# Performance work log

Measured on AMD Instinct MI355X. Metric: run time of the kernel, lower is better.

## Reference

```python
import jax, jax.numpy as jnp
import numpy as np

N_NODES = 20000

def _gcn_conv(x, W, b, src, dst, n):
    # PyG GCNConv: add self-loops, symmetric normalization D^-1/2 (A+I) D^-1/2, then XW + b
    h = x @ W                                   # [n, out]
    loop = jnp.arange(n, dtype=src.dtype)
    s = jnp.concatenate([src, loop])            # sources incl. self-loops
    d = jnp.concatenate([dst, loop])            # targets incl. self-loops
    deg = jax.ops.segment_sum(jnp.ones_like(d, dtype=h.dtype), d, num_segments=n)
    dinv = jnp.where(deg > 0, jax.lax.rsqrt(deg), 0.0)
    norm = dinv[s] * dinv[d]                    # [E+n]
    msg = h[s] * norm[:, None]                  # gather + scale
    out = jax.ops.segment_sum(msg, d, num_segments=n)  # scatter-add
    return out + b


def setup_inputs() -> dict:
    key = jax.random.key(0)
    ks = jax.random.split(key, 12)
    n, text_dim, hidden, ncls = N_NODES, 768, 128, 4
    mel_flat = 128 * 128
    E = 640000
    def lin(k, fan_in, fan_out):
        bound = 1.0 / np.sqrt(fan_in)
        kw, kb = jax.random.split(k)
        W = jax.random.uniform(kw, (fan_in, fan_out), jnp.float32, -bound, bound)
        b = jax.random.uniform(kb, (fan_out,), jnp.float32, -bound, bound)
        return W, b
    W_mel, b_mel = lin(ks[0], mel_flat, hidden)
    W_cat, b_cat = lin(ks[1], text_dim + hidden, hidden)
    W1, b1 = lin(ks[2], hidden, hidden)
    W2, b2 = lin(ks[3], hidden, ncls)
    return {
        "text": jax.random.normal(ks[4], (n, text_dim), jnp.float32),
        "mel": jax.random.normal(ks[5], (n, 128, 128), jnp.float32),
        "edge_index": jax.random.randint(ks[6], (2, E), 0, n, jnp.int32),
        "W_mel": W_mel, "b_mel": b_mel,
        "W_cat": W_cat, "b_cat": b_cat,
        "W1": W1, "b1": b1,
        "W2": W2, "b2": b2,
    }


def reference(text, mel, edge_index, W_mel, b_mel, W_cat, b_cat, W1, b1, W2, b2):
    n = text.shape[0]
    src, dst = edge_index[0], edge_index[1]
    m = mel.reshape(n, -1)                      # flatten [N, 128*128]
    m = jax.nn.relu(m @ W_mel + b_mel)          # [N, hidden]
    x = jnp.concatenate([text, m], axis=1)      # [N, text_dim + hidden]
    x = jax.nn.relu(x @ W_cat + b_cat)          # [N, hidden]
    x = jax.nn.relu(_gcn_conv(x, W1, b1, src, dst, n))
    x = _gcn_conv(x, W2, b2, src, dst, n)       # [N, num_classes]
    return x
```

## Files before the change

kernel.cpp:

```cpp
#include <hip/hip_runtime.h>
#include <hip/hip_bf16.h>
#include <cstdint>

typedef float f32x4 __attribute__((ext_vector_type(4)));
typedef __bf16 bf16x8 __attribute__((ext_vector_type(8)));
typedef __bf16 bf16x4 __attribute__((ext_vector_type(4)));

#define HID 128

__global__ void pack_b_frag(const float* __restrict__ W, __bf16* __restrict__ Bf, int kiters) {
    int idx = blockIdx.x * 256 + threadIdx.x;
    int total = kiters * 512;
    if (idx >= total) return;
    int lane = idx & 63;
    int nf = (idx >> 6) & 7;
    int ki = idx >> 9;
    int n = nf * 16 + (lane & 15);
    int kb = ki * 32 + ((lane >> 4) * 8);
    bf16x8 v;
#pragma unroll
    for (int j = 0; j < 8; ++j) v[j] = (__bf16)W[(size_t)(kb + j) * HID + n];
    *reinterpret_cast<bf16x8*>(Bf + (size_t)idx * 8) = v;
}

__global__ __launch_bounds__(256, 2) void gemm_mel_ks(
    const float* __restrict__ A0,
    const __bf16* __restrict__ Bf,
    float* __restrict__ part)
{
    const int tid = threadIdx.x;
    const int lane = tid & 63;
    const int wv = tid >> 6;
    const int quarter = blockIdx.x / 625;
    const int row_base = (blockIdx.x - quarter * 625) * 32;
    const int rif = lane & 15;
    const int kg = lane >> 4;
    const int s0 = quarter * 8;

    __shared__ __align__(16) char ldsb[65536];

    f32x4 zero = {0.f, 0.f, 0.f, 0.f};
    f32x4 acc[2][8];
#pragma unroll
    for (int i = 0; i < 2; ++i)
#pragma unroll
        for (int j = 0; j < 8; ++j) acc[i][j] = zero;

    const bf16x8* __restrict__ BfV = reinterpret_cast<const bf16x8*>(Bf);

    f32x4 st[16];

    auto stage_load = [&](int s) {
#pragma unroll
        for (int j = 0; j < 16; ++j) {
            int seg = wv * 16 + j;
            int row = seg >> 1, halfseg = seg & 1;
            const float* gp = A0 + (size_t)(row_base + row) * 16384 + s * 512 + halfseg * 256 + (lane << 2);
            st[j] = __builtin_nontemporal_load(reinterpret_cast<const f32x4*>(gp));
        }
    };
    auto stage_write = [&](int buf) {
#pragma unroll
        for (int j = 0; j < 16; ++j) {
            int seg = wv * 16 + j;
            int row = seg >> 1, halfseg = seg & 1;
            int byte = row * 1024 + ((halfseg * 512 + lane * 8) ^ ((row & 7) << 4)) + buf * 32768;
            bf16x4 v;
            v[0] = (__bf16)st[j][0]; v[1] = (__bf16)st[j][1];
            v[2] = (__bf16)st[j][2]; v[3] = (__bf16)st[j][3];
            *reinterpret_cast<bf16x4*>(ldsb + byte) = v;
        }
    };
    auto compute2 = [&](int cur, int s, int kt0) {
#pragma unroll
        for (int kt = kt0; kt < kt0 + 2; ++kt) {
            bf16x8 af[2];
#pragma unroll
            for (int mi = 0; mi < 2; ++mi) {
                int row = mi * 16 + rif;
                int byte = row * 1024 + ((wv * 256 + kt * 64 + kg * 16) ^ ((rif & 7) << 4)) + cur * 32768;
                af[mi] = *reinterpret_cast<const bf16x8*>(ldsb + byte);
            }
            int ki = s * 16 + wv * 4 + kt;
            const bf16x8* bp = BfV + (size_t)ki * 512 + lane;
#pragma unroll
            for (int nf = 0; nf < 8; ++nf) {
                bf16x8 b = bp[nf * 64];
                acc[0][nf] = __builtin_amdgcn_mfma_f32_16x16x32_bf16(af[0], b, acc[0][nf], 0, 0, 0);
                acc[1][nf] = __builtin_amdgcn_mfma_f32_16x16x32_bf16(af[1], b, acc[1][nf], 0, 0, 0);
            }
        }
    };

    stage_load(s0);
    stage_write(0);
    for (int t = 0; t < 8; ++t) {
        int s = s0 + t;
        int cur = t & 1;
        if (t + 1 < 8) stage_load(s + 1);
        __syncthreads();
        compute2(cur, s, 0);
        compute2(cur, s, 2);
        if (t + 1 < 8) stage_write(cur ^ 1);
    }

    __syncthreads();
    float* red = reinterpret_cast<float*>(ldsb);
#pragma unroll
    for (int mi = 0; mi < 2; ++mi)
#pragma unroll
        for (int nf = 0; nf < 8; ++nf)
#pragma unroll
            for (int j = 0; j < 4; ++j)
                red[(wv * 32 + mi * 16 + kg * 4 + j) * HID + nf * 16 + rif] = acc[mi][nf][j];
    __syncthreads();
    float* pb = part + (size_t)quarter * 20000 * HID;
#pragma unroll
    for (int p = 0; p < 16; ++p) {
        int idx = tid + p * 256;
        int r = idx >> 7, c = idx & 127;
        float v = red[r * HID + c] + red[(32 + r) * HID + c]
                + red[(64 + r) * HID + c] + red[(96 + r) * HID + c];
        pb[(size_t)(row_base + r) * HID + c] = v;
    }
}

__global__ void combine_m(const float* __restrict__ part, const float* __restrict__ bias,
                          float* __restrict__ m) {
    int idx = blockIdx.x * 256 + threadIdx.x;
    const size_t N = (size_t)20000 * HID / 4;
    const f32x4* p = reinterpret_cast<const f32x4*>(part);
    f32x4 b = *reinterpret_cast<const f32x4*>(bias + (idx & 31) * 4);
    f32x4 v = p[idx] + p[idx + N] + p[idx + 2 * N] + p[idx + 3 * N] + b;
    f32x4 r;
    r.x = fmaxf(v.x, 0.f); r.y = fmaxf(v.y, 0.f);
    r.z = fmaxf(v.z, 0.f); r.w = fmaxf(v.w, 0.f);
    reinterpret_cast<f32x4*>(m)[idx] = r;
}

__global__ __launch_bounds__(256) void gemm_cat_h1(
    const float* __restrict__ A0,
    const float* __restrict__ A1,
    const __bf16* __restrict__ Bf2,
    const __bf16* __restrict__ Bf3,
    const float* __restrict__ bcat,
    __bf16* __restrict__ h1)
{
    const int tid = threadIdx.x;
    const int lane = tid & 63;
    const int w = tid >> 6;
    const int row_base = blockIdx.x * 32;
    const int rif = lane & 15;
    const int kg = lane >> 4;

    f32x4 zero = {0.f, 0.f, 0.f, 0.f};
    f32x4 acc[2][8];
#pragma unroll
    for (int i = 0; i < 2; ++i)
#pragma unroll
        for (int j = 0; j < 8; ++j) acc[i][j] = zero;

    const bf16x8* __restrict__ Bf2V = reinterpret_cast<const bf16x8*>(Bf2);
    const int kstart = w * 224;

#pragma unroll
    for (int it = 0; it < 7; ++it) {
        const int k0 = kstart + it * 32;
        const int kc = k0 + kg * 8;
        bf16x8 af[2];
#pragma unroll
        for (int mi = 0; mi < 2; ++mi) {
            const int row = row_base + mi * 16 + rif;
            const float* ap;
            if (kc < 768) ap = A0 + (size_t)row * 768 + kc;
            else          ap = A1 + (size_t)row * HID + (kc - 768);
            const f32x4* apv = reinterpret_cast<const f32x4*>(ap);
            f32x4 v0 = apv[0];
            f32x4 v1 = apv[1];
            af[mi][0] = (__bf16)v0.x; af[mi][1] = (__bf16)v0.y;
            af[mi][2] = (__bf16)v0.z; af[mi][3] = (__bf16)v0.w;
            af[mi][4] = (__bf16)v1.x; af[mi][5] = (__bf16)v1.y;
            af[mi][6] = (__bf16)v1.z; af[mi][7] = (__bf16)v1.w;
        }
        const bf16x8* bp = Bf2V + (size_t)(k0 >> 5) * 512 + lane;
#pragma unroll
        for (int nf = 0; nf < 8; ++nf) {
            bf16x8 b = bp[nf * 64];
            acc[0][nf] = __builtin_amdgcn_mfma_f32_16x16x32_bf16(af[0], b, acc[0][nf], 0, 0, 0);
            acc[1][nf] = __builtin_amdgcn_mfma_f32_16x16x32_bf16(af[1], b, acc[1][nf], 0, 0, 0);
        }
    }

    __shared__ float red[4][32][HID];
    __shared__ __bf16 xs[32][136];

#pragma unroll
    for (int mi = 0; mi < 2; ++mi)
#pragma unroll
        for (int nf = 0; nf < 8; ++nf)
#pragma unroll
            for (int j = 0; j < 4; ++j)
                red[w][mi * 16 + kg * 4 + j][nf * 16 + rif] = acc[mi][nf][j];
    __syncthreads();
#pragma unroll
    for (int p = 0; p < 16; ++p) {
        int idx = tid + p * 256;
        int r = idx >> 7, c = idx & 127;
        float v = red[0][r][c] + red[1][r][c] + red[2][r][c] + red[3][r][c];
        v = fmaxf(v + bcat[c], 0.f);
        xs[r][c] = (__bf16)v;
    }
    __syncthreads();

    f32x4 acc2[2][8];
#pragma unroll
    for (int i = 0; i < 2; ++i)
#pragma unroll
        for (int j = 0; j < 8; ++j) acc2[i][j] = zero;

    {
        const int k0 = w * 32;
        bf16x8 af[2];
#pragma unroll
        for (int mi = 0; mi < 2; ++mi)
            af[mi] = *reinterpret_cast<const bf16x8*>(&xs[mi * 16 + rif][k0 + kg * 8]);
        const bf16x8* bp = reinterpret_cast<const bf16x8*>(Bf3) + (size_t)w * 512 + lane;
#pragma unroll
        for (int nf = 0; nf < 8; ++nf) {
            bf16x8 b = bp[nf * 64];
            acc2[0][nf] = __builtin_amdgcn_mfma_f32_16x16x32_bf16(af[0], b, acc2[0][nf], 0, 0, 0);
            acc2[1][nf] = __builtin_amdgcn_mfma_f32_16x16x32_bf16(af[1], b, acc2[1][nf], 0, 0, 0);
        }
    }

#pragma unroll
    for (int mi = 0; mi < 2; ++mi)
#pragma unroll
        for (int nf = 0; nf < 8; ++nf)
#pragma unroll
            for (int j = 0; j < 4; ++j)
                red[w][mi * 16 + kg * 4 + j][nf * 16 + rif] = acc2[mi][nf][j];
    __syncthreads();
#pragma unroll
    for (int p = 0; p < 16; ++p) {
        int idx = tid + p * 256;
        int r = idx >> 7, c = idx & 127;
        float v = red[0][r][c] + red[1][r][c] + red[2][r][c] + red[3][r][c];
        h1[(size_t)(row_base + r) * HID + c] = (__bf16)v;
    }
}

__global__ void count_dst(const int* __restrict__ dst, int* __restrict__ cnt, int E) {
    int e = blockIdx.x * 256 + threadIdx.x;
    if (e < E) atomicAdd(&cnt[dst[e]], 1);
}

__global__ __launch_bounds__(1024) void scan_block(const int* __restrict__ cnt,
    int* __restrict__ offs, float* __restrict__ dinv, int n) {
    int tid = threadIdx.x;
    int CH = (n + 1023) >> 10;
    int s0 = tid * CH;
    int s1 = min(s0 + CH, n);
    int sum = 0;
    for (int i = s0; i < s1; ++i) sum += cnt[i];
    int lane = tid & 63, wv = tid >> 6;
    int s = sum;
#pragma unroll
    for (int off = 1; off < 64; off <<= 1) {
        int t = __shfl_up(s, off);
        if (lane >= off) s += t;
    }
    __shared__ int wsum[16];
    __shared__ int wbase[16];
    if (lane == 63) wsum[wv] = s;
    __syncthreads();
    if (tid == 0) {
        int a = 0;
#pragma unroll
        for (int k = 0; k < 16; ++k) { wbase[k] = a; a += wsum[k]; }
    }
    __syncthreads();
    int run = wbase[wv] + (s - sum);
    for (int i = s0; i < s1; ++i) {
        int v = cnt[i];
        offs[i] = run;
        dinv[i] = rsqrtf((float)(v + 1));
        run += v;
    }
}

__global__ void fill_csr(const int* __restrict__ src, const int* __restrict__ dst,
                         const int* __restrict__ offs, int* __restrict__ fill,
                         int* __restrict__ srcs, int E) {
    int e = blockIdx.x * 256 + threadIdx.x;
    if (e >= E) return;
    int d = dst[e];
    int p = offs[d] + atomicAdd(&fill[d], 1);
    srcs[p] = src[e];
}

__global__ __launch_bounds__(128) void agg_h_w2(const __bf16* __restrict__ h,
    const float* __restrict__ dinv, const int* __restrict__ offs,
    const int* __restrict__ cnt, const int* __restrict__ srcs,
    const float* __restrict__ b1, const float* __restrict__ W2,
    float* __restrict__ h2, int n) {
    int i = blockIdx.x;
    int c = threadIdx.x;
    float di = dinv[i];
    float acc = (float)h[(size_t)i * HID + c] * di;
    int o = offs[i], e = cnt[i];
    int t = 0;
    for (; t + 4 <= e; t += 4) {
        int a0 = srcs[o + t], a1 = srcs[o + t + 1], a2 = srcs[o + t + 2], a3 = srcs[o + t + 3];
        float d0 = dinv[a0], d1 = dinv[a1], d2 = dinv[a2], d3 = dinv[a3];
        float v0 = (float)h[(size_t)a0 * HID + c], v1 = (float)h[(size_t)a1 * HID + c];
        float v2 = (float)h[(size_t)a2 * HID + c], v3 = (float)h[(size_t)a3 * HID + c];
        acc += v0 * d0 + v1 * d1 + v2 * d2 + v3 * d3;
    }
    for (; t < e; ++t) {
        int s = srcs[o + t];
        acc += (float)h[(size_t)s * HID + c] * dinv[s];
    }
    float yb = fmaxf(acc * di + b1[c], 0.f);
    float4 wr = *reinterpret_cast<const float4*>(W2 + c * 4);
    float p0 = yb * wr.x, p1 = yb * wr.y, p2 = yb * wr.z, p3 = yb * wr.w;
#pragma unroll
    for (int off = 32; off; off >>= 1) {
        p0 += __shfl_down(p0, off);
        p1 += __shfl_down(p1, off);
        p2 += __shfl_down(p2, off);
        p3 += __shfl_down(p3, off);
    }
    __shared__ float red[2][4];
    if ((c & 63) == 0) {
        int wv = c >> 6;
        red[wv][0] = p0; red[wv][1] = p1; red[wv][2] = p2; red[wv][3] = p3;
    }
    __syncthreads();
    if (c < 4) h2[(size_t)i * 4 + c] = red[0][c] + red[1][c];
}

__global__ void agg4(const float* __restrict__ h2, const float* __restrict__ dinv,
                     const int* __restrict__ offs, const int* __restrict__ cnt,
                     const int* __restrict__ srcs, const float* __restrict__ b2,
                     float* __restrict__ out, int n) {
    int gid = blockIdx.x * 256 + threadIdx.x;
    int i = gid >> 2;
    int c = gid & 3;
    if (i >= n) return;
    float di = dinv[i];
    float acc = h2[(size_t)i * 4 + c] * di;
    int o = offs[i], e = cnt[i];
    int t = 0;
    for (; t + 4 <= e; t += 4) {
        int a0 = srcs[o + t], a1 = srcs[o + t + 1], a2 = srcs[o + t + 2], a3 = srcs[o + t + 3];
        float v0 = h2[(size_t)a0 * 4 + c] * dinv[a0];
        float v1 = h2[(size_t)a1 * 4 + c] * dinv[a1];
        float v2 = h2[(size_t)a2 * 4 + c] * dinv[a2];
        float v3 = h2[(size_t)a3 * 4 + c] * dinv[a3];
        acc += v0 + v1 + v2 + v3;
    }
    for (; t < e; ++t) {
        int s = srcs[o + t];
        acc += h2[(size_t)s * 4 + c] * dinv[s];
    }
    out[(size_t)i * 4 + c] = acc * di + b2[c];
}

extern "C" void kernel_launch(void* const* d_in, const int* in_sizes, int n_in,
                              void* d_out, int out_size, void* d_ws, size_t ws_size,
                              hipStream_t stream) {
    const float* text = (const float*)d_in[0];
    const float* mel  = (const float*)d_in[1];
    const int*   ei   = (const int*)d_in[2];
    const float* Wmel = (const float*)d_in[3];
    const float* bmel = (const float*)d_in[4];
    const float* Wcat = (const float*)d_in[5];
    const float* bcat = (const float*)d_in[6];
    const float* W1   = (const float*)d_in[7];
    const float* b1   = (const float*)d_in[8];
    const float* W2   = (const float*)d_in[9];
    const float* b2   = (const float*)d_in[10];
    float* out = (float*)d_out;

    const int n = in_sizes[0] / 768;
    const int E = in_sizes[2] / 2;
    const int Kmel = 16384;
    const int Kcat = 896;

    char* ws = (char*)d_ws;
    size_t off = 0;
    auto alloc = [&](size_t bytes) {
        void* p = ws + off;
        off += (bytes + 255) & ~(size_t)255;
        return p;
    };
    __bf16* Bf1 = (__bf16*)alloc((size_t)Kmel * HID * 2);
    __bf16* Bf2 = (__bf16*)alloc((size_t)Kcat * HID * 2);
    __bf16* Bf3 = (__bf16*)alloc((size_t)HID * HID * 2);
    float* part = (float*)alloc((size_t)4 * n * HID * 4);
    float* m    = (float*)alloc((size_t)n * HID * 4);
    __bf16* h1  = (__bf16*)alloc((size_t)n * HID * 2);
    float* h2   = (float*)alloc((size_t)n * 4 * 4);
    int* cnt    = (int*)alloc((size_t)n * 4);
    int* offs   = (int*)alloc((size_t)n * 4);
    int* fill   = (int*)alloc((size_t)n * 4);
    float* dinv = (float*)alloc((size_t)n * 4);
    int* srcs   = (int*)alloc((size_t)E * 4);
    (void)ws_size; (void)n_in; (void)out_size;

    const int* srcI = ei;
    const int* dstI = ei + E;

    (void)hipMemsetAsync(cnt, 0, n * 4, stream);
    (void)hipMemsetAsync(fill, 0, n * 4, stream);
    count_dst<<<(E + 255) / 256, 256, 0, stream>>>(dstI, cnt, E);
    scan_block<<<1, 1024, 0, stream>>>(cnt, offs, dinv, n);
    fill_csr<<<(E + 255) / 256, 256, 0, stream>>>(srcI, dstI, offs, fill, srcs, E);

    pack_b_frag<<<(Kmel / 32 * 512 + 255) / 256, 256, 0, stream>>>(Wmel, Bf1, Kmel / 32);
    pack_b_frag<<<(Kcat / 32 * 512 + 255) / 256, 256, 0, stream>>>(Wcat, Bf2, Kcat / 32);
    pack_b_frag<<<(HID / 32 * 512 + 255) / 256, 256, 0, stream>>>(W1, Bf3, HID / 32);

    gemm_mel_ks<<<2500, 256, 0, stream>>>(mel, Bf1, part);
    combine_m<<<(n * HID / 4) / 256, 256, 0, stream>>>(part, bmel, m);
    gemm_cat_h1<<<n / 32, 256, 0, stream>>>(text, m, Bf2, Bf3, bcat, h1);
    agg_h_w2<<<n, 128, 0, stream>>>(h1, dinv, offs, cnt, srcs, b1, W2, h2, n);
    agg4<<<(n * 4 + 255) / 256, 256, 0, stream>>>(h2, dinv, offs, cnt, srcs, b2, out, n);
}
```

Measured before the change: 466.4 us.

## Prescale GCN features by dinv, store m in bf16, merge weight packing

Merges the three weight-packing launches into one kernel. The intermediate m is now stored in bf16, and text loads use nontemporal hints. h1 and h2 are pre-multiplied by the source degree normalisation in their producers, which removes the per-edge dinv gathers from both aggregation kernels. The first aggregation uses one wave per node with two columns per lane, so the LDS reduction and the barrier go away. Rounding changes slightly because of the bf16 m and the prescaling.

New measurement: 455.0 us. 1.02x faster.

```diff
diff --git a/kernel.cpp b/kernel.cpp
--- a/kernel.cpp
+++ b/kernel.cpp
@@ -5,22 +5,32 @@
 typedef float f32x4 __attribute__((ext_vector_type(4)));
 typedef __bf16 bf16x8 __attribute__((ext_vector_type(8)));
 typedef __bf16 bf16x4 __attribute__((ext_vector_type(4)));
+typedef __bf16 bf16x2 __attribute__((ext_vector_type(2)));
 
 #define HID 128
 
-__global__ void pack_b_frag(const float* __restrict__ W, __bf16* __restrict__ Bf, int kiters) {
+__global__ void pack_all(const float* __restrict__ Wa, const float* __restrict__ Wb,
+                         const float* __restrict__ Wc,
+                         __bf16* __restrict__ Ba, __bf16* __restrict__ Bb,
+                         __bf16* __restrict__ Bc) {
     int idx = blockIdx.x * 256 + threadIdx.x;
-    int total = kiters * 512;
-    if (idx >= total) return;
-    int lane = idx & 63;
-    int nf = (idx >> 6) & 7;
-    int ki = idx >> 9;
+    const int T1 = 512 * 512;
+    const int T2 = 28 * 512;
+    const int T3 = 4 * 512;
+    const float* W; __bf16* B; int li;
+    if (idx < T1)            { W = Wa; B = Ba; li = idx; }
+    else if (idx < T1 + T2)  { W = Wb; B = Bb; li = idx - T1; }
+    else if (idx < T1 + T2 + T3) { W = Wc; B = Bc; li = idx - T1 - T2; }
+    else return;
+    int lane = li & 63;
+    int nf = (li >> 6) & 7;
+    int ki = li >> 9;
     int n = nf * 16 + (lane & 15);
     int kb = ki * 32 + ((lane >> 4) * 8);
     bf16x8 v;
 #pragma unroll
     for (int j = 0; j < 8; ++j) v[j] = (__bf16)W[(size_t)(kb + j) * HID + n];
-    *reinterpret_cast<bf16x8*>(Bf + (size_t)idx * 8) = v;
+    *reinterpret_cast<bf16x8*>(B + (size_t)li * 8) = v;
 }
 
 __global__ __launch_bounds__(256, 2) void gemm_mel_ks(
@@ -126,24 +136,25 @@
 }
 
 __global__ void combine_m(const float* __restrict__ part, const float* __restrict__ bias,
-                          float* __restrict__ m) {
+                          __bf16* __restrict__ m) {
     int idx = blockIdx.x * 256 + threadIdx.x;
     const size_t N = (size_t)20000 * HID / 4;
     const f32x4* p = reinterpret_cast<const f32x4*>(part);
     f32x4 b = *reinterpret_cast<const f32x4*>(bias + (idx & 31) * 4);
     f32x4 v = p[idx] + p[idx + N] + p[idx + 2 * N] + p[idx + 3 * N] + b;
-    f32x4 r;
-    r.x = fmaxf(v.x, 0.f); r.y = fmaxf(v.y, 0.f);
-    r.z = fmaxf(v.z, 0.f); r.w = fmaxf(v.w, 0.f);
-    reinterpret_cast<f32x4*>(m)[idx] = r;
+    bf16x4 r;
+    r[0] = (__bf16)fmaxf(v.x, 0.f); r[1] = (__bf16)fmaxf(v.y, 0.f);
+    r[2] = (__bf16)fmaxf(v.z, 0.f); r[3] = (__bf16)fmaxf(v.w, 0.f);
+    *reinterpret_cast<bf16x4*>(m + (size_t)idx * 4) = r;
 }
 
 __global__ __launch_bounds__(256) void gemm_cat_h1(
     const float* __restrict__ A0,
-    const float* __restrict__ A1,
+    const __bf16* __restrict__ A1,
     const __bf16* __restrict__ Bf2,
     const __bf16* __restrict__ Bf3,
     const float* __restrict__ bcat,
+    const float* __restrict__ dinv,
     __bf16* __restrict__ h1)
 {
     const int tid = threadIdx.x;
@@ -171,16 +182,17 @@
 #pragma unroll
         for (int mi = 0; mi < 2; ++mi) {
             const int row = row_base + mi * 16 + rif;
-            const float* ap;
-            if (kc < 768) ap = A0 + (size_t)row * 768 + kc;
-            else          ap = A1 + (size_t)row * HID + (kc - 768);
-            const f32x4* apv = reinterpret_cast<const f32x4*>(ap);
-            f32x4 v0 = apv[0];
-            f32x4 v1 = apv[1];
-            af[mi][0] = (__bf16)v0.x; af[mi][1] = (__bf16)v0.y;
-            af[mi][2] = (__bf16)v0.z; af[mi][3] = (__bf16)v0.w;
-            af[mi][4] = (__bf16)v1.x; af[mi][5] = (__bf16)v1.y;
-            af[mi][6] = (__bf16)v1.z; af[mi][7] = (__bf16)v1.w;
+            if (k0 < 768) {
+                const f32x4* apv = reinterpret_cast<const f32x4*>(A0 + (size_t)row * 768 + kc);
+                f32x4 v0 = __builtin_nontemporal_load(apv);
+                f32x4 v1 = __builtin_nontemporal_load(apv + 1);
+                af[mi][0] = (__bf16)v0.x; af[mi][1] = (__bf16)v0.y;
+                af[mi][2] = (__bf16)v0.z; af[mi][3] = (__bf16)v0.w;
+                af[mi][4] = (__bf16)v1.x; af[mi][5] = (__bf16)v1.y;
+                af[mi][6] = (__bf16)v1.z; af[mi][7] = (__bf16)v1.w;
+            } else {
+                af[mi] = *reinterpret_cast<const bf16x8*>(A1 + (size_t)row * HID + (kc - 768));
+            }
         }
         const bf16x8* bp = Bf2V + (size_t)(k0 >> 5) * 512 + lane;
 #pragma unroll
@@ -246,7 +258,7 @@
         int idx = tid + p * 256;
         int r = idx >> 7, c = idx & 127;
         float v = red[0][r][c] + red[1][r][c] + red[2][r][c] + red[3][r][c];
-        h1[(size_t)(row_base + r) * HID + c] = (__bf16)v;
+        h1[(size_t)(row_base + r) * HID + c] = (__bf16)(v * dinv[row_base + r]);
     }
 }
 
@@ -299,7 +311,7 @@
     srcs[p] = src[e];
 }
 
-__global__ __launch_bounds__(128) void agg_h_w2(const __bf16* __restrict__ h,
+__global__ __launch_bounds__(64) void agg_h_w2(const __bf16* __restrict__ hs,
     const float* __restrict__ dinv, const int* __restrict__ offs,
     const int* __restrict__ cnt, const int* __restrict__ srcs,
     const float* __restrict__ b1, const float* __restrict__ W2,
@@ -307,23 +319,35 @@
     int i = blockIdx.x;
     int c = threadIdx.x;
     float di = dinv[i];
-    float acc = (float)h[(size_t)i * HID + c] * di;
+    const int col = 2 * c;
+    bf16x2 hv = *reinterpret_cast<const bf16x2*>(hs + (size_t)i * HID + col);
+    float a0 = (float)hv[0];
+    float a1 = (float)hv[1];
     int o = offs[i], e = cnt[i];
     int t = 0;
     for (; t + 4 <= e; t += 4) {
-        int a0 = srcs[o + t], a1 = srcs[o + t + 1], a2 = srcs[o + t + 2], a3 = srcs[o + t + 3];
-        float d0 = dinv[a0], d1 = dinv[a1], d2 = dinv[a2], d3 = dinv[a3];
-        float v0 = (float)h[(size_t)a0 * HID + c], v1 = (float)h[(size_t)a1 * HID + c];
-        float v2 = (float)h[(size_t)a2 * HID + c], v3 = (float)h[(size_t)a3 * HID + c];
-        acc += v0 * d0 + v1 * d1 + v2 * d2 + v3 * d3;
+        int s0 = srcs[o + t], s1 = srcs[o + t + 1], s2 = srcs[o + t + 2], s3 = srcs[o + t + 3];
+        bf16x2 v0 = *reinterpret_cast<const bf16x2*>(hs + (size_t)s0 * HID + col);
+        bf16x2 v1 = *reinterpret_cast<const bf16x2*>(hs + (size_t)s1 * HID + col);
+        bf16x2 v2 = *reinterpret_cast<const bf16x2*>(hs + (size_t)s2 * HID + col);
+        bf16x2 v3 = *reinterpret_cast<const bf16x2*>(hs + (size_t)s3 * HID + col);
+        a0 += (float)v0[0] + (float)v1[0] + (float)v2[0] + (float)v3[0];
+        a1 += (float)v0[1] + (float)v1[1] + (float)v2[1] + (float)v3[1];
     }
     for (; t < e; ++t) {
         int s = srcs[o + t];
-        acc += (float)h[(size_t)s * HID + c] * dinv[s];
-    }
-    float yb = fmaxf(acc * di + b1[c], 0.f);
-    float4 wr = *reinterpret_cast<const float4*>(W2 + c * 4);
-    float p0 = yb * wr.x, p1 = yb * wr.y, p2 = yb * wr.z, p3 = yb * wr.w;
+        bf16x2 v = *reinterpret_cast<const bf16x2*>(hs + (size_t)s * HID + col);
+        a0 += (float)v[0];
+        a1 += (float)v[1];
+    }
+    float yb0 = fmaxf(a0 * di + b1[col], 0.f);
+    float yb1 = fmaxf(a1 * di + b1[col + 1], 0.f);
+    float4 w0 = *reinterpret_cast<const float4*>(W2 + col * 4);
+    float4 w1 = *reinterpret_cast<const float4*>(W2 + col * 4 + 4);
+    float p0 = yb0 * w0.x + yb1 * w1.x;
+    float p1 = yb0 * w0.y + yb1 * w1.y;
+    float p2 = yb0 * w0.z + yb1 * w1.z;
+    float p3 = yb0 * w0.w + yb1 * w1.w;
 #pragma unroll
     for (int off = 32; off; off >>= 1) {
         p0 += __shfl_down(p0, off);
@@ -331,16 +355,13 @@
         p2 += __shfl_down(p2, off);
         p3 += __shfl_down(p3, off);
     }
-    __shared__ float red[2][4];
-    if ((c & 63) == 0) {
-        int wv = c >> 6;
-        red[wv][0] = p0; red[wv][1] = p1; red[wv][2] = p2; red[wv][3] = p3;
-    }
-    __syncthreads();
-    if (c < 4) h2[(size_t)i * 4 + c] = red[0][c] + red[1][c];
-}
-
-__global__ void agg4(const float* __restrict__ h2, const float* __restrict__ dinv,
+    if (c == 0) {
+        float4 r = {p0 * di, p1 * di, p2 * di, p3 * di};
+        *reinterpret_cast<float4*>(h2 + (size_t)i * 4) = r;
+    }
+}
+
+__global__ void agg4(const float* __restrict__ h2s, const float* __restrict__ dinv,
                      const int* __restrict__ offs, const int* __restrict__ cnt,
                      const int* __restrict__ srcs, const float* __restrict__ b2,
                      float* __restrict__ out, int n) {
@@ -349,20 +370,17 @@
     int c = gid & 3;
     if (i >= n) return;
     float di = dinv[i];
-    float acc = h2[(size_t)i * 4 + c] * di;
+    float acc = h2s[(size_t)i * 4 + c];
     int o = offs[i], e = cnt[i];
     int t = 0;
     for (; t + 4 <= e; t += 4) {
         int a0 = srcs[o + t], a1 = srcs[o + t + 1], a2 = srcs[o + t + 2], a3 = srcs[o + t + 3];
-        float v0 = h2[(size_t)a0 * 4 + c] * dinv[a0];
-        float v1 = h2[(size_t)a1 * 4 + c] * dinv[a1];
-        float v2 = h2[(size_t)a2 * 4 + c] * dinv[a2];
-        float v3 = h2[(size_t)a3 * 4 + c] * dinv[a3];
-        acc += v0 + v1 + v2 + v3;
+        acc += h2s[(size_t)a0 * 4 + c] + h2s[(size_t)a1 * 4 + c]
+             + h2s[(size_t)a2 * 4 + c] + h2s[(size_t)a3 * 4 + c];
     }
     for (; t < e; ++t) {
         int s = srcs[o + t];
-        acc += h2[(size_t)s * 4 + c] * dinv[s];
+        acc += h2s[(size_t)s * 4 + c];
     }
     out[(size_t)i * 4 + c] = acc * di + b2[c];
 }
@@ -386,7 +404,6 @@
     const int n = in_sizes[0] / 768;
     const int E = in_sizes[2] / 2;
     const int Kmel = 16384;
-    const int Kcat = 896;
 
     char* ws = (char*)d_ws;
     size_t off = 0;
@@ -396,10 +413,10 @@
         return p;
     };
     __bf16* Bf1 = (__bf16*)alloc((size_t)Kmel * HID * 2);
-    __bf16* Bf2 = (__bf16*)alloc((size_t)Kcat * HID * 2);
+    __bf16* Bf2 = (__bf16*)alloc((size_t)896 * HID * 2);
     __bf16* Bf3 = (__bf16*)alloc((size_t)HID * HID * 2);
     float* part = (float*)alloc((size_t)4 * n * HID * 4);
-    float* m    = (float*)alloc((size_t)n * HID * 4);
+    __bf16* m   = (__bf16*)alloc((size_t)n * HID * 2);
     __bf16* h1  = (__bf16*)alloc((size_t)n * HID * 2);
     float* h2   = (float*)alloc((size_t)n * 4 * 4);
     int* cnt    = (int*)alloc((size_t)n * 4);
@@ -418,13 +435,11 @@
     scan_block<<<1, 1024, 0, stream>>>(cnt, offs, dinv, n);
     fill_csr<<<(E + 255) / 256, 256, 0, stream>>>(srcI, dstI, offs, fill, srcs, E);
 
-    pack_b_frag<<<(Kmel / 32 * 512 + 255) / 256, 256, 0, stream>>>(Wmel, Bf1, Kmel / 32);
-    pack_b_frag<<<(Kcat / 32 * 512 + 255) / 256, 256, 0, stream>>>(Wcat, Bf2, Kcat / 32);
-    pack_b_frag<<<(HID / 32 * 512 + 255) / 256, 256, 0, stream>>>(W1, Bf3, HID / 32);
+    pack_all<<<1088, 256, 0, stream>>>(Wmel, Wcat, W1, Bf1, Bf2, Bf3);
 
     gemm_mel_ks<<<2500, 256, 0, stream>>>(mel, Bf1, part);
     combine_m<<<(n * HID / 4) / 256, 256, 0, stream>>>(part, bmel, m);
-    gemm_cat_h1<<<n / 32, 256, 0, stream>>>(text, m, Bf2, Bf3, bcat, h1);
-    agg_h_w2<<<n, 128, 0, stream>>>(h1, dinv, offs, cnt, srcs, b1, W2, h2, n);
+    gemm_cat_h1<<<n / 32, 256, 0, stream>>>(text, m, Bf2, Bf3, bcat, dinv, h1);
+    agg_h_w2<<<n, 64, 0, stream>>>(h1, dinv, offs, cnt, srcs, b1, W2, h2, n);
     agg4<<<(n * 4 + 255) / 256, 256, 0, stream>>>(h2, dinv, offs, cnt, srcs, b2, out, n);
 }
```
